# Kernel optimization log

Measured on AMD Instinct MI355X. Metric: run time of the kernel, lower is better.

## Reference

```python
import jax, jax.numpy as jnp
import numpy as np

N_NODES = 100000
N_EDGES = 3200000
IN_DIM, HID_DIM, OUT_DIM = 512, 32, 16


def spmm(rows, cols, vals, dense):
    # out[r] = sum_{e: rows[e]==r} vals[e] * dense[cols[e]]  == adj @ dense (COO)
    gathered = vals[:, None] * dense[cols]          # [E, D]
    return jax.ops.segment_sum(gathered, rows, num_segments=N_NODES)


def gcn_layer(x, adj_rows, adj_cols, adj_vals, W):
    support = x @ W                                  # dense mm [N, out]
    return spmm(adj_rows, adj_cols, adj_vals, support)


def setup_inputs() -> dict:
    key = jax.random.key(0)
    ks = jax.random.split(key, 8)
    x = jax.random.normal(ks[0], (N_NODES, IN_DIM), dtype=jnp.float32)
    adj_rows = jax.random.randint(ks[1], (N_EDGES,), 0, N_NODES, dtype=jnp.int32)
    adj_cols = jax.random.randint(ks[2], (N_EDGES,), 0, N_NODES, dtype=jnp.int32)
    adj_vals = jax.random.uniform(ks[3], (N_EDGES,), dtype=jnp.float32)
    W1 = jax.random.normal(ks[4], (IN_DIM, HID_DIM), dtype=jnp.float32)
    W2 = jax.random.normal(ks[5], (HID_DIM, OUT_DIM), dtype=jnp.float32)
    W3 = jax.random.normal(ks[6], (OUT_DIM, HID_DIM), dtype=jnp.float32)
    W4 = jax.random.normal(ks[7], (HID_DIM, IN_DIM), dtype=jnp.float32)
    return {"x": x, "adj_rows": adj_rows, "adj_cols": adj_cols,
            "adj_vals": adj_vals, "W1": W1, "W2": W2, "W3": W3, "W4": W4}


def reference(x, adj_rows, adj_cols, adj_vals, W1, W2, W3, W4):
    encoded1 = gcn_layer(x, adj_rows, adj_cols, adj_vals, W1)        # [N, 32]
    encoded2 = gcn_layer(encoded1, adj_rows, adj_cols, adj_vals, W2) # [N, 16]
    decoded1 = gcn_layer(encoded2, adj_rows, adj_cols, adj_vals, W3) # [N, 32]
    decoded2 = gcn_layer(decoded1, adj_rows, adj_cols, adj_vals, W4) # [N, 512]
    return (decoded2, encoded2)
```

## Files before the change

### kernel.cpp

```cpp
#include <hip/hip_runtime.h>
#include <hip/hip_bf16.h>


#define N_NODES 100000
#define N_EDGES 3200000
#define RPB_LOG 7
#define RPB (1 << RPB_LOG)
#define NB ((N_NODES + RPB - 1) / RPB)
#define CHUNK 16384
#define NCHUNK ((N_EDGES + CHUNK - 1) / CHUNK)
#define EPT (CHUNK / 512)

typedef __attribute__((ext_vector_type(4))) float f32x4;
typedef __attribute__((ext_vector_type(8))) short s16x8;
typedef __attribute__((ext_vector_type(4))) unsigned short u16x4;
typedef __attribute__((ext_vector_type(4))) int i32x4;

static __device__ inline s16x8 cvt8(const float4& lo, const float4& hi) {
  unsigned p0, p1, p2, p3;
  asm("v_cvt_pk_bf16_f32 %0, %1, %2" : "=v"(p0) : "v"(lo.x), "v"(lo.y));
  asm("v_cvt_pk_bf16_f32 %0, %1, %2" : "=v"(p1) : "v"(lo.z), "v"(lo.w));
  asm("v_cvt_pk_bf16_f32 %0, %1, %2" : "=v"(p2) : "v"(hi.x), "v"(hi.y));
  asm("v_cvt_pk_bf16_f32 %0, %1, %2" : "=v"(p3) : "v"(hi.z), "v"(hi.w));
  i32x4 pi = {(int)p0, (int)p1, (int)p2, (int)p3};
  return __builtin_bit_cast(s16x8, pi);
}

static __device__ inline unsigned pk2(float a, float b) {
  unsigned p;
  asm("v_cvt_pk_bf16_f32 %0, %1, %2" : "=v"(p) : "v"(a), "v"(b));
  return p;
}
static __device__ inline float b2f(unsigned short u) {
  return __uint_as_float(((unsigned)u) << 16);
}

__global__ __launch_bounds__(256) void wconv12_kernel(
    const float* __restrict__ W1, const float* __restrict__ W2,
    uint4* __restrict__ Wfrag) {
  int s = blockIdx.x * 256 + threadIdx.x;
  if (s >= 1024) return;
  int lane = s & 63, kt = s >> 6;
  int n = lane & 15;
  int kb = kt * 32 + (lane >> 4) * 8;
  unsigned p[4];
#pragma unroll
  for (int i = 0; i < 4; ++i) {
    float lo = 0.f, hi = 0.f;
#pragma unroll
    for (int m = 0; m < 32; ++m) {
      float w2 = W2[m * 16 + n];
      lo += W1[(kb + 2 * i) * 32 + m] * w2;
      hi += W1[(kb + 2 * i + 1) * 32 + m] * w2;
    }
    p[i] = pk2(lo, hi);
  }
  Wfrag[s] = make_uint4(p[0], p[1], p[2], p[3]);
}

__global__ __launch_bounds__(256) void mm1_kernel(
    const float* __restrict__ x, const uint4* __restrict__ Wfrag,
    unsigned short* __restrict__ out) {
  const int t = threadIdx.x;
  const int lane = t & 63;
  const int w = t >> 6;
  const int rbase = blockIdx.x * 128 + w * 32;
  const int lrow = lane & 15;
  const int kg = lane >> 4;

  int r0c = rbase + lrow;       if (r0c > N_NODES - 1) r0c = N_NODES - 1;
  int r1c = rbase + 16 + lrow;  if (r1c > N_NODES - 1) r1c = N_NODES - 1;
  const float* xp0 = x + (size_t)r0c * 512 + kg * 8;
  const float* xp1 = x + (size_t)r1c * 512 + kg * 8;
  const s16x8* Wf = (const s16x8*)Wfrag;

  f32x4 acc0 = {0.f, 0.f, 0.f, 0.f}, acc1 = {0.f, 0.f, 0.f, 0.f};

#pragma unroll 4
  for (int kt = 0; kt < 16; ++kt) {
    float4 a0lo = *(const float4*)(xp0 + kt * 32);
    float4 a0hi = *(const float4*)(xp0 + kt * 32 + 4);
    float4 a1lo = *(const float4*)(xp1 + kt * 32);
    float4 a1hi = *(const float4*)(xp1 + kt * 32 + 4);
    s16x8 b = Wf[kt * 64 + lane];
    s16x8 a0 = cvt8(a0lo, a0hi);
    s16x8 a1 = cvt8(a1lo, a1hi);
    acc0 = __builtin_amdgcn_mfma_f32_16x16x32_bf16(a0, b, acc0, 0, 0, 0);
    acc1 = __builtin_amdgcn_mfma_f32_16x16x32_bf16(a1, b, acc1, 0, 0, 0);
  }

  const int col = lane & 15;
#pragma unroll
  for (int reg = 0; reg < 4; ++reg) {
    int r0 = rbase + kg * 4 + reg;
    if (r0 < N_NODES)
      out[(size_t)r0 * 16 + col] = (unsigned short)(pk2(acc0[reg], acc0[reg]) & 0xFFFF);
    int r1 = rbase + 16 + kg * 4 + reg;
    if (r1 < N_NODES)
      out[(size_t)r1 * 16 + col] = (unsigned short)(pk2(acc1[reg], acc1[reg]) & 0xFFFF);
  }
}

__global__ __launch_bounds__(512) void localsort_kernel(
    const int* __restrict__ rows, const int* __restrict__ cols,
    const float* __restrict__ vals, int2* __restrict__ cv_loc,
    int* __restrict__ ofs, int* __restrict__ gcnt) {
  __shared__ int lcnt[NB];
  __shared__ int lofs[NB + 1];
  __shared__ int ssum[512];
  const int c = blockIdx.x, t = threadIdx.x;
  const int c0 = c * CHUNK, c1 = min(c0 + CHUNK, N_EDGES);

  for (int i = t; i < NB; i += 512) lcnt[i] = 0;
  __syncthreads();

  int rr[EPT];
#pragma unroll
  for (int u = 0; u < EPT; ++u) {
    int e = c0 + t + u * 512;
    rr[u] = (e < c1) ? rows[e] : -1;
    if (rr[u] >= 0) atomicAdd(&lcnt[rr[u] >> RPB_LOG], 1);
  }
  __syncthreads();

  int v0 = (2 * t < NB) ? lcnt[2 * t] : 0;
  int v1 = (2 * t + 1 < NB) ? lcnt[2 * t + 1] : 0;
  if (v0) atomicAdd(&gcnt[2 * t], v0);
  if (v1) atomicAdd(&gcnt[2 * t + 1], v1);
  ssum[t] = v0 + v1;
  __syncthreads();
  for (int off = 1; off < 512; off <<= 1) {
    int xv = (t >= off) ? ssum[t - off] : 0;
    __syncthreads();
    ssum[t] += xv;
    __syncthreads();
  }
  int excl = (t == 0) ? 0 : ssum[t - 1];
  if (2 * t < NB) lofs[2 * t] = excl;
  if (2 * t + 1 < NB) lofs[2 * t + 1] = excl + v0;
  if (t == 511) lofs[NB] = ssum[511];
  __syncthreads();

  for (int i = t; i <= NB; i += 512) ofs[c * (NB + 1) + i] = lofs[i];
  for (int i = t; i < NB; i += 512) lcnt[i] = 0;
  __syncthreads();

#pragma unroll
  for (int u = 0; u < EPT; ++u) {
    int r = rr[u];
    if (r >= 0) {
      int e = c0 + t + u * 512;
      int b = r >> RPB_LOG;
      int rank = atomicAdd(&lcnt[b], 1);
      cv_loc[c0 + lofs[b] + rank] =
          make_int2(((r & (RPB - 1)) << 17) | cols[e], __float_as_int(vals[e]));
    }
  }
}

__global__ __launch_bounds__(1024) void scan782_kernel(
    const int* __restrict__ gcnt, int* __restrict__ bstart,
    int* __restrict__ row_ptr) {
  __shared__ int s[1024];
  int t = threadIdx.x;
  int v = (t < NB) ? gcnt[t] : 0;
  s[t] = v;
  __syncthreads();
  for (int off = 1; off < 1024; off <<= 1) {
    int xv = (t >= off) ? s[t - off] : 0;
    __syncthreads();
    s[t] += xv;
    __syncthreads();
  }
  if (t < NB) bstart[t] = s[t] - v;
  if (t == 0) { bstart[NB] = N_EDGES; row_ptr[N_NODES] = N_EDGES; }
}

__global__ __launch_bounds__(256) void refine4_kernel(
    const int* __restrict__ ofs, const int* __restrict__ bstart,
    const int2* __restrict__ cv_loc, unsigned* __restrict__ cv_csr,
    int* __restrict__ row_ptr) {
  __shared__ int gs[NCHUNK];
  __shared__ int q[NCHUNK + 1];
  __shared__ int sq[256];
  __shared__ int rcnt[RPB];
  __shared__ int rbase[RPB];
  const int b = blockIdx.x, t = threadIdx.x;

  int cnt_t = 0;
  if (t < NCHUNK) {
    int g0 = ofs[t * (NB + 1) + b];
    int g1 = ofs[t * (NB + 1) + b + 1];
    gs[t] = t * CHUNK + g0;
    cnt_t = g1 - g0;
  }
  sq[t] = cnt_t;
  __syncthreads();
  for (int off = 1; off < 256; off <<= 1) {
    int v = (t >= off) ? sq[t - off] : 0;
    __syncthreads();
    sq[t] += v;
    __syncthreads();
  }
  if (t < NCHUNK) q[t] = sq[t] - cnt_t;
  if (t == 0) q[NCHUNK] = sq[255];
  if (t < RPB) rcnt[t] = 0;
  __syncthreads();
  const int Q = q[NCHUNK];

  int lo = 0;
  for (int i = t; i < Q; i += 256) {
    while (q[lo + 1] <= i) ++lo;
    int2 e = cv_loc[gs[lo] + (i - q[lo])];
    atomicAdd(&rcnt[e.x >> 17], 1);
  }
  __syncthreads();

  int rv = (t < RPB) ? rcnt[t] : 0;
  sq[t] = rv;
  __syncthreads();
  for (int off = 1; off < RPB; off <<= 1) {
    int v = (t >= off && t < RPB) ? sq[t - off] : 0;
    __syncthreads();
    if (t < RPB) sq[t] += v;
    __syncthreads();
  }
  if (t < RPB) {
    int base = bstart[b] + sq[t] - rv;
    rbase[t] = base;
    int gr = (b << RPB_LOG) + t;
    if (gr < N_NODES) row_ptr[gr] = base;
    rcnt[t] = 0;
  }
  __syncthreads();

  lo = 0;
  for (int i = t; i < Q; i += 256) {
    while (q[lo + 1] <= i) ++lo;
    int2 e = cv_loc[gs[lo] + (i - q[lo])];
    int rl = e.x >> 17;
    int rank = atomicAdd(&rcnt[rl], 1);
    float v = __int_as_float(e.y);
    unsigned vb = pk2(v, v);
    cv_csr[rbase[rl] + rank] =
        ((unsigned)(e.x & 0x1FFFF) << 15) | (vb & 0x7FFF);
  }
}

template <int OM>
__global__ __launch_bounds__(256) void spmm_b16_kernel(
    const int* __restrict__ rp, const unsigned* __restrict__ colval,
    const unsigned short* __restrict__ in, unsigned short* __restrict__ outb,
    float* __restrict__ outf) {
  const int t = threadIdx.x;
  const int r = blockIdx.x * 64 + (t >> 2);
  const int q = t & 3;
  if (r >= N_NODES) return;
  const int k0 = rp[r], k1 = rp[r + 1];
  float a0 = 0.f, a1 = 0.f, a2 = 0.f, a3 = 0.f;

  int k = k0;
  for (; k + 7 < k1; k += 8) {
    unsigned cv[8];
#pragma unroll
    for (int u = 0; u < 8; ++u) cv[u] = colval[k + u];
    u16x4 g[8];
#pragma unroll
    for (int u = 0; u < 8; ++u)
      g[u] = *(const u16x4*)(in + (size_t)(cv[u] >> 15) * 16 + q * 4);
#pragma unroll
    for (int u = 0; u < 8; ++u) {
      float v = __uint_as_float((cv[u] & 0x7FFF) << 16);
      a0 += v * b2f(g[u][0]);
      a1 += v * b2f(g[u][1]);
      a2 += v * b2f(g[u][2]);
      a3 += v * b2f(g[u][3]);
    }
  }
  for (; k + 1 < k1; k += 2) {
    unsigned ca = colval[k], cb = colval[k + 1];
    u16x4 ga = *(const u16x4*)(in + (size_t)(ca >> 15) * 16 + q * 4);
    u16x4 gb = *(const u16x4*)(in + (size_t)(cb >> 15) * 16 + q * 4);
    float va = __uint_as_float((ca & 0x7FFF) << 16);
    float vb = __uint_as_float((cb & 0x7FFF) << 16);
    a0 += va * b2f(ga[0]); a1 += va * b2f(ga[1]);
    a2 += va * b2f(ga[2]); a3 += va * b2f(ga[3]);
    a0 += vb * b2f(gb[0]); a1 += vb * b2f(gb[1]);
    a2 += vb * b2f(gb[2]); a3 += vb * b2f(gb[3]);
  }
  if (k < k1) {
    unsigned cv = colval[k];
    u16x4 g = *(const u16x4*)(in + (size_t)(cv >> 15) * 16 + q * 4);
    float v = __uint_as_float((cv & 0x7FFF) << 16);
    a0 += v * b2f(g[0]); a1 += v * b2f(g[1]);
    a2 += v * b2f(g[2]); a3 += v * b2f(g[3]);
  }

  uint2 pk = make_uint2(pk2(a0, a1), pk2(a2, a3));
  *(uint2*)(outb + (size_t)r * 16 + q * 4) = pk;
  if (OM == 1) {
    *(float4*)(outf + (size_t)r * 16 + q * 4) = make_float4(a0, a1, a2, a3);
  }
}

__global__ __launch_bounds__(256) void spmm_dec_kernel(
    const int* __restrict__ rp, const unsigned* __restrict__ colval,
    const unsigned short* __restrict__ in, const float* __restrict__ W3,
    const float* __restrict__ W4, float* __restrict__ out) {
  __shared__ float t3s[64][20];
  const int t = threadIdx.x;
  const int r0 = blockIdx.x * 64;
  const int lr = t >> 2;
  const int q = t & 3;
  const int r = r0 + lr;

  float w4a[32], w4b[32];
#pragma unroll
  for (int m = 0; m < 32; ++m) {
    w4a[m] = W4[m * 512 + t];
    w4b[m] = W4[m * 512 + t + 256];
  }
  float wa[16], wb[16];
#pragma unroll
  for (int kk = 0; kk < 16; ++kk) {
    float sa = 0.f, sb = 0.f;
#pragma unroll
    for (int m = 0; m < 32; ++m) {
      float w3 = W3[kk * 32 + m];
      sa += w3 * w4a[m];
      sb += w3 * w4b[m];
    }
    wa[kk] = sa;
    wb[kk] = sb;
  }

  float a0 = 0.f, a1 = 0.f, a2 = 0.f, a3 = 0.f;
  if (r < N_NODES) {
    const int k0 = rp[r], k1 = rp[r + 1];
    int k = k0;
    for (; k + 7 < k1; k += 8) {
      unsigned cv[8];
#pragma unroll
      for (int u = 0; u < 8; ++u) cv[u] = colval[k + u];
      u16x4 g[8];
#pragma unroll
      for (int u = 0; u < 8; ++u)
        g[u] = *(const u16x4*)(in + (size_t)(cv[u] >> 15) * 16 + q * 4);
#pragma unroll
      for (int u = 0; u < 8; ++u) {
        float v = __uint_as_float((cv[u] & 0x7FFF) << 16);
        a0 += v * b2f(g[u][0]);
        a1 += v * b2f(g[u][1]);
        a2 += v * b2f(g[u][2]);
        a3 += v * b2f(g[u][3]);
      }
    }
    for (; k < k1; ++k) {
      unsigned cv = colval[k];
      u16x4 g = *(const u16x4*)(in + (size_t)(cv >> 15) * 16 + q * 4);
      float v = __uint_as_float((cv & 0x7FFF) << 16);
      a0 += v * b2f(g[0]); a1 += v * b2f(g[1]);
      a2 += v * b2f(g[2]); a3 += v * b2f(g[3]);
    }
  }
  t3s[lr][q * 4 + 0] = a0;
  t3s[lr][q * 4 + 1] = a1;
  t3s[lr][q * 4 + 2] = a2;
  t3s[lr][q * 4 + 3] = a3;
  __syncthreads();

  const int nrows = min(64, N_NODES - r0);
  for (int rr = 0; rr < nrows; ++rr) {
    float4 c0 = *(const float4*)&t3s[rr][0];
    float4 c1 = *(const float4*)&t3s[rr][4];
    float4 c2 = *(const float4*)&t3s[rr][8];
    float4 c3 = *(const float4*)&t3s[rr][12];
    float sa = c0.x * wa[0] + c0.y * wa[1] + c0.z * wa[2] + c0.w * wa[3]
             + c1.x * wa[4] + c1.y * wa[5] + c1.z * wa[6] + c1.w * wa[7]
             + c2.x * wa[8] + c2.y * wa[9] + c2.z * wa[10] + c2.w * wa[11]
             + c3.x * wa[12] + c3.y * wa[13] + c3.z * wa[14] + c3.w * wa[15];
    float sb = c0.x * wb[0] + c0.y * wb[1] + c0.z * wb[2] + c0.w * wb[3]
             + c1.x * wb[4] + c1.y * wb[5] + c1.z * wb[6] + c1.w * wb[7]
             + c2.x * wb[8] + c2.y * wb[9] + c2.z * wb[10] + c2.w * wb[11]
             + c3.x * wb[12] + c3.y * wb[13] + c3.z * wb[14] + c3.w * wb[15];
    float* o = out + (size_t)(r0 + rr) * 512;
    o[t] = sa;
    o[t + 256] = sb;
  }
}

extern "C" void kernel_launch(void* const* d_in, const int* in_sizes, int n_in,
                              void* d_out, int out_size, void* d_ws, size_t ws_size,
                              hipStream_t stream) {
  const float* x     = (const float*)d_in[0];
  const int*   arows = (const int*)d_in[1];
  const int*   acols = (const int*)d_in[2];
  const float* avals = (const float*)d_in[3];
  const float* W1    = (const float*)d_in[4];
  const float* W2    = (const float*)d_in[5];
  const float* W3    = (const float*)d_in[6];
  const float* W4    = (const float*)d_in[7];

  float* out = (float*)d_out;
  float* dec = out;
  float* enc = out + (size_t)N_NODES * 512;

  unsigned short* bh  = (unsigned short*)d_ws;
  unsigned short* bu  = bh + (size_t)N_NODES * 16;
  unsigned short* be  = bu + (size_t)N_NODES * 16;
  unsigned* cv_csr  = (unsigned*)(be + (size_t)N_NODES * 16);
  int*      row_ptr = (int*)(cv_csr + N_EDGES);

  int2*  cv_loc = (int2*)dec;
  uint4* Wfrag  = (uint4*)(cv_loc + N_EDGES);
  int*   ofs    = (int*)(Wfrag + 1024);
  int*   bstart = ofs + NCHUNK * (NB + 1);
  int*   gcnt   = bstart + NB + 1;

  hipMemsetAsync(gcnt, 0, NB * sizeof(int), stream);
  wconv12_kernel<<<4, 256, 0, stream>>>(W1, W2, Wfrag);
  localsort_kernel<<<NCHUNK, 512, 0, stream>>>(arows, acols, avals, cv_loc, ofs, gcnt);
  scan782_kernel<<<1, 1024, 0, stream>>>(gcnt, bstart, row_ptr);
  refine4_kernel<<<NB, 256, 0, stream>>>(ofs, bstart, cv_loc, cv_csr, row_ptr);

  const int spGrid = (N_NODES + 63) / 64;
  mm1_kernel<<<(N_NODES + 127) / 128, 256, 0, stream>>>(x, Wfrag, bh);
  spmm_b16_kernel<0><<<spGrid, 256, 0, stream>>>(row_ptr, cv_csr, bh, bu, nullptr);
  spmm_b16_kernel<1><<<spGrid, 256, 0, stream>>>(row_ptr, cv_csr, bu, be, enc);
  spmm_b16_kernel<0><<<spGrid, 256, 0, stream>>>(row_ptr, cv_csr, be, bh, nullptr);
  spmm_dec_kernel<<<spGrid, 256, 0, stream>>>(row_ptr, cv_csr, bh, W3, W4, dec);
}
```

Before: 372.2 us.

## Split each row's edges across two thread groups and fold block scan into refine

Each row in the SpMM and decoder kernels is now processed by 8 threads instead of 4. Two 4-thread halves each sum half the row's edges, and the halves are combined with a cross-lane shuffle. This doubles the number of gather streams in flight per row to hide memory latency, at the cost of half as many rows per block and extra shuffles. The separate single-block scan kernel is removed: each refine block now sums the preceding bucket counts itself. This saves one launch but adds a redundant partial reduction in every block. The bounds checks are dropped because N_NODES divides evenly by 32.

```diff
diff --git a/kernel.cpp b/kernel.cpp
--- a/kernel.cpp
+++ b/kernel.cpp
@@ -158,26 +158,8 @@
   }
 }
 
-__global__ __launch_bounds__(1024) void scan782_kernel(
-    const int* __restrict__ gcnt, int* __restrict__ bstart,
-    int* __restrict__ row_ptr) {
-  __shared__ int s[1024];
-  int t = threadIdx.x;
-  int v = (t < NB) ? gcnt[t] : 0;
-  s[t] = v;
-  __syncthreads();
-  for (int off = 1; off < 1024; off <<= 1) {
-    int xv = (t >= off) ? s[t - off] : 0;
-    __syncthreads();
-    s[t] += xv;
-    __syncthreads();
-  }
-  if (t < NB) bstart[t] = s[t] - v;
-  if (t == 0) { bstart[NB] = N_EDGES; row_ptr[N_NODES] = N_EDGES; }
-}
-
-__global__ __launch_bounds__(256) void refine4_kernel(
-    const int* __restrict__ ofs, const int* __restrict__ bstart,
+__global__ __launch_bounds__(256) void refine5_kernel(
+    const int* __restrict__ ofs, const int* __restrict__ gcnt,
     const int2* __restrict__ cv_loc, unsigned* __restrict__ cv_csr,
     int* __restrict__ row_ptr) {
   __shared__ int gs[NCHUNK];
@@ -185,7 +167,19 @@
   __shared__ int sq[256];
   __shared__ int rcnt[RPB];
   __shared__ int rbase[RPB];
+  __shared__ int bstart_s;
   const int b = blockIdx.x, t = threadIdx.x;
+
+  int part = 0;
+  for (int i = t; i < b; i += 256) part += gcnt[i];
+  sq[t] = part;
+  __syncthreads();
+  for (int off = 128; off > 0; off >>= 1) {
+    if (t < off) sq[t] += sq[t + off];
+    __syncthreads();
+  }
+  if (t == 0) bstart_s = sq[0];
+  __syncthreads();
 
   int cnt_t = 0;
   if (t < NCHUNK) {
@@ -226,12 +220,13 @@
     __syncthreads();
   }
   if (t < RPB) {
-    int base = bstart[b] + sq[t] - rv;
+    int base = bstart_s + sq[t] - rv;
     rbase[t] = base;
     int gr = (b << RPB_LOG) + t;
     if (gr < N_NODES) row_ptr[gr] = base;
     rcnt[t] = 0;
   }
+  if (b == 0 && t == 0) row_ptr[N_NODES] = N_EDGES;
   __syncthreads();
 
   lo = 0;
@@ -253,14 +248,16 @@
     const unsigned short* __restrict__ in, unsigned short* __restrict__ outb,
     float* __restrict__ outf) {
   const int t = threadIdx.x;
-  const int r = blockIdx.x * 64 + (t >> 2);
+  const int r = blockIdx.x * 32 + (t >> 3);
   const int q = t & 3;
-  if (r >= N_NODES) return;
+  const int hh = (t >> 2) & 1;
   const int k0 = rp[r], k1 = rp[r + 1];
+  const int len0 = (k1 - k0 + 1) >> 1;
+  int k = k0 + hh * len0;
+  const int ke = hh ? k1 : (k0 + len0);
   float a0 = 0.f, a1 = 0.f, a2 = 0.f, a3 = 0.f;
 
-  int k = k0;
-  for (; k + 7 < k1; k += 8) {
+  for (; k + 7 < ke; k += 8) {
     unsigned cv[8];
 #pragma unroll
     for (int u = 0; u < 8; ++u) cv[u] = colval[k + u];
@@ -277,18 +274,24 @@
       a3 += v * b2f(g[u][3]);
     }
   }
-  for (; k + 1 < k1; k += 2) {
-    unsigned ca = colval[k], cb = colval[k + 1];
-    u16x4 ga = *(const u16x4*)(in + (size_t)(ca >> 15) * 16 + q * 4);
-    u16x4 gb = *(const u16x4*)(in + (size_t)(cb >> 15) * 16 + q * 4);
-    float va = __uint_as_float((ca & 0x7FFF) << 16);
-    float vb = __uint_as_float((cb & 0x7FFF) << 16);
-    a0 += va * b2f(ga[0]); a1 += va * b2f(ga[1]);
-    a2 += va * b2f(ga[2]); a3 += va * b2f(ga[3]);
-    a0 += vb * b2f(gb[0]); a1 += vb * b2f(gb[1]);
-    a2 += vb * b2f(gb[2]); a3 += vb * b2f(gb[3]);
-  }
-  if (k < k1) {
+  for (; k + 3 < ke; k += 4) {
+    unsigned cv[4];
+#pragma unroll
+    for (int u = 0; u < 4; ++u) cv[u] = colval[k + u];
+    u16x4 g[4];
+#pragma unroll
+    for (int u = 0; u < 4; ++u)
+      g[u] = *(const u16x4*)(in + (size_t)(cv[u] >> 15) * 16 + q * 4);
+#pragma unroll
+    for (int u = 0; u < 4; ++u) {
+      float v = __uint_as_float((cv[u] & 0x7FFF) << 16);
+      a0 += v * b2f(g[u][0]);
+      a1 += v * b2f(g[u][1]);
+      a2 += v * b2f(g[u][2]);
+      a3 += v * b2f(g[u][3]);
+    }
+  }
+  for (; k < ke; ++k) {
     unsigned cv = colval[k];
     u16x4 g = *(const u16x4*)(in + (size_t)(cv >> 15) * 16 + q * 4);
     float v = __uint_as_float((cv & 0x7FFF) << 16);
@@ -296,10 +299,16 @@
     a2 += v * b2f(g[2]); a3 += v * b2f(g[3]);
   }
 
-  uint2 pk = make_uint2(pk2(a0, a1), pk2(a2, a3));
-  *(uint2*)(outb + (size_t)r * 16 + q * 4) = pk;
-  if (OM == 1) {
-    *(float4*)(outf + (size_t)r * 16 + q * 4) = make_float4(a0, a1, a2, a3);
+  a0 += __shfl_xor(a0, 4);
+  a1 += __shfl_xor(a1, 4);
+  a2 += __shfl_xor(a2, 4);
+  a3 += __shfl_xor(a3, 4);
+
+  if (hh == 0) {
+    uint2 pk = make_uint2(pk2(a0, a1), pk2(a2, a3));
+    *(uint2*)(outb + (size_t)r * 16 + q * 4) = pk;
+    if (OM == 1)
+      *(float4*)(outf + (size_t)r * 16 + q * 4) = make_float4(a0, a1, a2, a3);
   }
 }
 
@@ -307,70 +316,88 @@
     const int* __restrict__ rp, const unsigned* __restrict__ colval,
     const unsigned short* __restrict__ in, const float* __restrict__ W3,
     const float* __restrict__ W4, float* __restrict__ out) {
-  __shared__ float t3s[64][20];
+  __shared__ float t3s[32][20];
   const int t = threadIdx.x;
-  const int r0 = blockIdx.x * 64;
-  const int lr = t >> 2;
+  const int r0 = blockIdx.x * 32;
+  const int lr = t >> 3;
   const int q = t & 3;
+  const int hh = (t >> 2) & 1;
   const int r = r0 + lr;
 
-  float w4a[32], w4b[32];
+  float wa[16], wb[16];
+#pragma unroll
+  for (int kk = 0; kk < 16; ++kk) { wa[kk] = 0.f; wb[kk] = 0.f; }
 #pragma unroll
   for (int m = 0; m < 32; ++m) {
-    w4a[m] = W4[m * 512 + t];
-    w4b[m] = W4[m * 512 + t + 256];
-  }
-  float wa[16], wb[16];
-#pragma unroll
-  for (int kk = 0; kk < 16; ++kk) {
-    float sa = 0.f, sb = 0.f;
-#pragma unroll
-    for (int m = 0; m < 32; ++m) {
+    float w4A = W4[m * 512 + t];
+    float w4B = W4[m * 512 + t + 256];
+#pragma unroll
+    for (int kk = 0; kk < 16; ++kk) {
       float w3 = W3[kk * 32 + m];
-      sa += w3 * w4a[m];
-      sb += w3 * w4b[m];
-    }
-    wa[kk] = sa;
-    wb[kk] = sb;
-  }
-
+      wa[kk] += w3 * w4A;
+      wb[kk] += w3 * w4B;
+    }
+  }
+
+  const int k0 = rp[r], k1 = rp[r + 1];
+  const int len0 = (k1 - k0 + 1) >> 1;
+  int k = k0 + hh * len0;
+  const int ke = hh ? k1 : (k0 + len0);
   float a0 = 0.f, a1 = 0.f, a2 = 0.f, a3 = 0.f;
-  if (r < N_NODES) {
-    const int k0 = rp[r], k1 = rp[r + 1];
-    int k = k0;
-    for (; k + 7 < k1; k += 8) {
-      unsigned cv[8];
-#pragma unroll
-      for (int u = 0; u < 8; ++u) cv[u] = colval[k + u];
-      u16x4 g[8];
-#pragma unroll
-      for (int u = 0; u < 8; ++u)
-        g[u] = *(const u16x4*)(in + (size_t)(cv[u] >> 15) * 16 + q * 4);
-#pragma unroll
-      for (int u = 0; u < 8; ++u) {
-        float v = __uint_as_float((cv[u] & 0x7FFF) << 16);
-        a0 += v * b2f(g[u][0]);
-        a1 += v * b2f(g[u][1]);
-        a2 += v * b2f(g[u][2]);
-        a3 += v * b2f(g[u][3]);
-      }
-    }
-    for (; k < k1; ++k) {
-      unsigned cv = colval[k];
-      u16x4 g = *(const u16x4*)(in + (size_t)(cv >> 15) * 16 + q * 4);
-      float v = __uint_as_float((cv & 0x7FFF) << 16);
-      a0 += v * b2f(g[0]); a1 += v * b2f(g[1]);
-      a2 += v * b2f(g[2]); a3 += v * b2f(g[3]);
-    }
-  }
-  t3s[lr][q * 4 + 0] = a0;
-  t3s[lr][q * 4 + 1] = a1;
-  t3s[lr][q * 4 + 2] = a2;
-  t3s[lr][q * 4 + 3] = a3;
-  __syncthreads();
-
-  const int nrows = min(64, N_NODES - r0);
-  for (int rr = 0; rr < nrows; ++rr) {
+  for (; k + 7 < ke; k += 8) {
+    unsigned cv[8];
+#pragma unroll
+    for (int u = 0; u < 8; ++u) cv[u] = colval[k + u];
+    u16x4 g[8];
+#pragma unroll
+    for (int u = 0; u < 8; ++u)
+      g[u] = *(const u16x4*)(in + (size_t)(cv[u] >> 15) * 16 + q * 4);
+#pragma unroll
+    for (int u = 0; u < 8; ++u) {
+      float v = __uint_as_float((cv[u] & 0x7FFF) << 16);
+      a0 += v * b2f(g[u][0]);
+      a1 += v * b2f(g[u][1]);
+      a2 += v * b2f(g[u][2]);
+      a3 += v * b2f(g[u][3]);
+    }
+  }
+  for (; k + 3 < ke; k += 4) {
+    unsigned cv[4];
+#pragma unroll
+    for (int u = 0; u < 4; ++u) cv[u] = colval[k + u];
+    u16x4 g[4];
+#pragma unroll
+    for (int u = 0; u < 4; ++u)
+      g[u] = *(const u16x4*)(in + (size_t)(cv[u] >> 15) * 16 + q * 4);
+#pragma unroll
+    for (int u = 0; u < 4; ++u) {
+      float v = __uint_as_float((cv[u] & 0x7FFF) << 16);
+      a0 += v * b2f(g[u][0]);
+      a1 += v * b2f(g[u][1]);
+      a2 += v * b2f(g[u][2]);
+      a3 += v * b2f(g[u][3]);
+    }
+  }
+  for (; k < ke; ++k) {
+    unsigned cv = colval[k];
+    u16x4 g = *(const u16x4*)(in + (size_t)(cv >> 15) * 16 + q * 4);
+    float v = __uint_as_float((cv & 0x7FFF) << 16);
+    a0 += v * b2f(g[0]); a1 += v * b2f(g[1]);
+    a2 += v * b2f(g[2]); a3 += v * b2f(g[3]);
+  }
+  a0 += __shfl_xor(a0, 4);
+  a1 += __shfl_xor(a1, 4);
+  a2 += __shfl_xor(a2, 4);
+  a3 += __shfl_xor(a3, 4);
+  if (hh == 0) {
+    t3s[lr][q * 4 + 0] = a0;
+    t3s[lr][q * 4 + 1] = a1;
+    t3s[lr][q * 4 + 2] = a2;
+    t3s[lr][q * 4 + 3] = a3;
+  }
+  __syncthreads();
+
+  for (int rr = 0; rr < 32; ++rr) {
     float4 c0 = *(const float4*)&t3s[rr][0];
     float4 c1 = *(const float4*)&t3s[rr][4];
     float4 c2 = *(const float4*)&t3s[rr][8];
@@ -414,16 +441,14 @@
   int2*  cv_loc = (int2*)dec;
   uint4* Wfrag  = (uint4*)(cv_loc + N_EDGES);
   int*   ofs    = (int*)(Wfrag + 1024);
-  int*   bstart = ofs + NCHUNK * (NB + 1);
-  int*   gcnt   = bstart + NB + 1;
+  int*   gcnt   = ofs + NCHUNK * (NB + 1);
 
   hipMemsetAsync(gcnt, 0, NB * sizeof(int), stream);
   wconv12_kernel<<<4, 256, 0, stream>>>(W1, W2, Wfrag);
   localsort_kernel<<<NCHUNK, 512, 0, stream>>>(arows, acols, avals, cv_loc, ofs, gcnt);
-  scan782_kernel<<<1, 1024, 0, stream>>>(gcnt, bstart, row_ptr);
-  refine4_kernel<<<NB, 256, 0, stream>>>(ofs, bstart, cv_loc, cv_csr, row_ptr);
-
-  const int spGrid = (N_NODES + 63) / 64;
+  refine5_kernel<<<NB, 256, 0, stream>>>(ofs, gcnt, cv_loc, cv_csr, row_ptr);
+
+  const int spGrid = N_NODES / 32;
   mm1_kernel<<<(N_NODES + 127) / 128, 256, 0, stream>>>(x, Wfrag, bh);
   spmm_b16_kernel<0><<<spGrid, 256, 0, stream>>>(row_ptr, cv_csr, bh, bu, nullptr);
   spmm_b16_kernel<1><<<spGrid, 256, 0, stream>>>(row_ptr, cv_csr, bu, be, enc);
```

Result: no change. 365.1 us (-1.9%).
